# Optimization experiments

Measured on AMD Instinct MI355X. Metric: run time of the kernel, lower is better.

## Reference

```python
import jax, jax.numpy as jnp
import numpy as np

N = 50000      # nodes
E = 600000     # edges
D = 128        # inp_dim == emb_dim
R = 100        # num_rels
B = 4          # num_bases
L = 2          # num_layers
EPS = 1e-5


def setup_inputs() -> dict:
    key = jax.random.key(0)
    ks = jax.random.split(key, 4 + 6 * L)
    inp = {
        "feat": jax.random.normal(ks[0], (N, D), dtype=jnp.float32),
        "src": jax.random.randint(ks[1], (E,), 0, N),
        "dst": jax.random.randint(ks[2], (E,), 0, N),
        "etype": jax.random.randint(ks[3], (E,), 0, R),
    }
    for l in range(L):
        o = 4 + 6 * l
        s = 1.0 / np.sqrt(D)
        inp[f"V{l}"] = jax.random.normal(ks[o + 0], (B, D, D), dtype=jnp.float32) * s
        inp[f"comb{l}"] = jax.random.normal(ks[o + 1], (R, B), dtype=jnp.float32)
        inp[f"loop{l}"] = jax.random.normal(ks[o + 2], (D, D), dtype=jnp.float32) * s
        inp[f"bias{l}"] = jax.random.normal(ks[o + 3], (D,), dtype=jnp.float32) * 0.01
        inp[f"gamma{l}"] = jnp.ones((D,), dtype=jnp.float32)
        inp[f"beta{l}"] = jnp.zeros((D,), dtype=jnp.float32)
    return inp


def _rel_graph_conv(x, src, dst, etype, V, comb, W_loop, bias):
    # basis-decomposed relational conv: W_r = sum_b comb[r,b] * V[b]
    xb = jnp.einsum('nd,bdo->nbo', x, V)            # [N, B, D] project onto bases once
    msg = jnp.einsum('ebo,eb->eo', xb[src], comb[etype])  # [E, D] per-edge typed message
    agg = jax.ops.segment_sum(msg, dst, num_segments=N)   # scatter-add to destinations
    h = agg + x @ W_loop + bias                     # self-loop + bias (DGL defaults)
    return jax.nn.relu(h)


def _batch_norm(h, gamma, beta):
    mu = jnp.mean(h, axis=0)
    var = jnp.mean(jnp.square(h - mu), axis=0)      # biased var (training-mode BN)
    return gamma * (h - mu) * jax.lax.rsqrt(var + EPS) + beta


def reference(feat, src, dst, etype,
              V0, comb0, loop0, bias0, gamma0, beta0,
              V1, comb1, loop1, bias1, gamma1, beta1):
    h = feat
    h = _rel_graph_conv(h, src, dst, etype, V0, comb0, loop0, bias0)
    h = _batch_norm(h, gamma0, beta0)
    h = _rel_graph_conv(h, src, dst, etype, V1, comb1, loop1, bias1)
    h = _batch_norm(h, gamma1, beta1)
    return h  # JK='last'
```

## Files before the change

### kernel.cpp

```cpp
#include <hip/hip_runtime.h>
#include <hip/hip_bf16.h>

#define Nn 50000
#define Ee 600000
#define Dd 128
#define EPSc 1e-5f
#define GX 391

typedef unsigned int u32;
typedef unsigned short u16;
typedef short s16x8 __attribute__((ext_vector_type(8)));
typedef float f32x4 __attribute__((ext_vector_type(4)));

__device__ inline float bf2f(u32 lo16) { return __uint_as_float(lo16 << 16); }
__device__ inline u16 f2bf(float f) {
    u32 b = __float_as_uint(f);
    return (u16)((b + 0x7fffu + ((b >> 16) & 1u)) >> 16);
}
__device__ inline void gload16(const void* g, void* l) {
    __builtin_amdgcn_global_load_lds(
        (const __attribute__((address_space(1))) u32*)g,
        (__attribute__((address_space(3))) u32*)l, 16, 0, 0);
}

__global__ __launch_bounds__(256) void hist_k(const int* __restrict__ dst,
                                              int* __restrict__ cnt) {
    int e = blockIdx.x * 256 + threadIdx.x;
    if (e < Ee) atomicAdd(&cnt[dst[e]], 1);
}

__global__ __launch_bounds__(1024) void scan_k(const int* __restrict__ cnt,
                                               int* __restrict__ rowp) {
    __shared__ int wsum[16];
    __shared__ int carry_s;
    const int t = threadIdx.x, lane = t & 63, w = t >> 6;
    if (t == 0) { carry_s = 0; rowp[0] = 0; }
    __syncthreads();
    for (int base = 0; base < Nn; base += 1024) {
        int v = (base + t < Nn) ? cnt[base + t] : 0;
        int incl = v;
#pragma unroll
        for (int off = 1; off < 64; off <<= 1) {
            int u = __shfl_up(incl, off, 64);
            if (lane >= off) incl += u;
        }
        if (lane == 63) wsum[w] = incl;
        __syncthreads();
        if (t == 0) {
            int run = carry_s;
#pragma unroll
            for (int i = 0; i < 16; i++) { int s = wsum[i]; wsum[i] = run; run += s; }
            carry_s = run;
        }
        __syncthreads();
        if (base + t < Nn) rowp[base + t + 1] = wsum[w] + incl;
        __syncthreads();
    }
}

__global__ __launch_bounds__(256) void scatter_k(const int* __restrict__ src,
                                                 const int* __restrict__ dst,
                                                 const int* __restrict__ et,
                                                 int* __restrict__ cursor,
                                                 int2* __restrict__ se) {
    int e = blockIdx.x * 256 + threadIdx.x;
    if (e < Ee) {
        int pos = atomicAdd(&cursor[dst[e]], 1);
        se[pos] = make_int2(src[e], et[e]);
    }
}

__global__ __launch_bounds__(256) void conv_k(const float* __restrict__ in,
                                              u16* __restrict__ out) {
    const int total = Nn * 32;
    for (int i = blockIdx.x * 256 + threadIdx.x; i < total; i += gridDim.x * 256) {
        float4 v = ((const float4*)in)[i];
        ((ushort4*)out)[i] = make_ushort4(f2bf(v.x), f2bf(v.y), f2bf(v.z), f2bf(v.w));
    }
}

__global__ __launch_bounds__(256) void wprep_k(const float* __restrict__ V,
                                               const float* __restrict__ loop,
                                               u16* __restrict__ Wt) {
    int i = blockIdx.x * 256 + threadIdx.x;
    if (i >= 128 * 640) return;
    int c = i / 640, k = i - c * 640;
    float v = (k < 512) ? V[(size_t)k * 128 + c] : loop[(size_t)(k - 512) * 128 + c];
    Wt[i] = f2bf(v);
}

__global__ __launch_bounds__(256) void agg_k(const u16* __restrict__ x16,
                                             const int2* __restrict__ se,
                                             const int* __restrict__ rowp,
                                             const float* __restrict__ comb,
                                             u16* __restrict__ yb16) {
    const int node = blockIdx.x * 4 + (threadIdx.x >> 6);
    const int lane = threadIdx.x & 63;
    const int beg = rowp[node], end = rowp[node + 1];
    float a0x = 0.f, a0y = 0.f, a1x = 0.f, a1y = 0.f;
    float a2x = 0.f, a2y = 0.f, a3x = 0.f, a3y = 0.f;
    const int eL = end - 1;
    const int co = lane * 2;

    for (int e0 = beg; e0 < end; e0 += 4) {
        const int m = end - e0;
        const int2 rc0 = se[e0];
        const int2 rc1 = se[min(e0 + 1, eL)];
        const int2 rc2 = se[min(e0 + 2, eL)];
        const int2 rc3 = se[min(e0 + 3, eL)];
        u32 x0 = *(const u32*)&x16[(size_t)rc0.x * 128 + co];
        u32 x1 = *(const u32*)&x16[(size_t)rc1.x * 128 + co];
        u32 x2 = *(const u32*)&x16[(size_t)rc2.x * 128 + co];
        u32 x3 = *(const u32*)&x16[(size_t)rc3.x * 128 + co];
        if (m < 4) x3 = 0;
        if (m < 3) x2 = 0;
        if (m < 2) x1 = 0;
        const float4 c0 = ((const float4*)comb)[rc0.y];
        const float4 c1 = ((const float4*)comb)[rc1.y];
        const float4 c2 = ((const float4*)comb)[rc2.y];
        const float4 c3 = ((const float4*)comb)[rc3.y];
#define ACC1(c, xv)                                        \
        {                                                  \
            const float fx = bf2f((xv) & 0xffffu);         \
            const float fy = bf2f((xv) >> 16);             \
            a0x += c.x * fx; a0y += c.x * fy;              \
            a1x += c.y * fx; a1y += c.y * fy;              \
            a2x += c.z * fx; a2y += c.z * fy;              \
            a3x += c.w * fx; a3y += c.w * fy;              \
        }
        ACC1(c0, x0)
        ACC1(c1, x1)
        ACC1(c2, x2)
        ACC1(c3, x3)
#undef ACC1
    }
    u32* yp = (u32*)(yb16 + (size_t)node * 512);
    yp[lane]       = (u32)f2bf(a0x) | ((u32)f2bf(a0y) << 16);
    yp[64 + lane]  = (u32)f2bf(a1x) | ((u32)f2bf(a1y) << 16);
    yp[128 + lane] = (u32)f2bf(a2x) | ((u32)f2bf(a2y) << 16);
    yp[192 + lane] = (u32)f2bf(a3x) | ((u32)f2bf(a3y) << 16);
}

__global__ __launch_bounds__(256) void gemm_mfma_k(const u16* __restrict__ yb16,
                                                   const u16* __restrict__ x16,
                                                   const u16* __restrict__ Wt,
                                                   const float* __restrict__ bias,
                                                   float* __restrict__ OUT,
                                                   float* __restrict__ partials) {
    __shared__ __align__(16) char As[8192];
    __shared__ __align__(16) char Bs[8192];
    const int tid = threadIdx.x;
    const int lane = tid & 63, wid = tid >> 6;
    const int wr = wid >> 1, wc = wid & 1;
    const int bm = blockIdx.x * 128;

    f32x4 acc[4][4] = {};

    const int r0 = wid * 32;
    const int lrow = lane >> 2;
    const int sphys = lane & 3;
    const int rowL0 = r0 + lrow, rowL1 = r0 + 16 + lrow;
    const int slog0 = (sphys ^ ((rowL0 >> 1) & 3)) * 8;
    const int slog1 = (sphys ^ ((rowL1 >> 1) & 3)) * 8;
    int ga0 = bm + rowL0; if (ga0 >= Nn) ga0 = Nn - 1;
    int ga1 = bm + rowL1; if (ga1 >= Nn) ga1 = Nn - 1;

    for (int k0 = 0; k0 < 640; k0 += 32) {
        __syncthreads();
        const u16 *as0, *as1;
        if (k0 < 512) {
            as0 = yb16 + (size_t)ga0 * 512 + k0 + slog0;
            as1 = yb16 + (size_t)ga1 * 512 + k0 + slog1;
        } else {
            as0 = x16 + (size_t)ga0 * 128 + (k0 - 512) + slog0;
            as1 = x16 + (size_t)ga1 * 128 + (k0 - 512) + slog1;
        }
        gload16(as0, &As[r0 * 64]);
        gload16(as1, &As[(r0 + 16) * 64]);
        gload16(Wt + (size_t)rowL0 * 640 + k0 + slog0, &Bs[r0 * 64]);
        gload16(Wt + (size_t)rowL1 * 640 + k0 + slog1, &Bs[(r0 + 16) * 64]);
        __syncthreads();
        s16x8 a[4], b[4];
#pragma unroll
        for (int m = 0; m < 4; m++) {
            int row = wr * 64 + m * 16 + (lane & 15);
            a[m] = *(const s16x8*)&As[row * 64 + (((lane >> 4) ^ ((row >> 1) & 3)) << 4)];
            int col = wc * 64 + m * 16 + (lane & 15);
            b[m] = *(const s16x8*)&Bs[col * 64 + (((lane >> 4) ^ ((col >> 1) & 3)) << 4)];
        }
#pragma unroll
        for (int m = 0; m < 4; m++)
#pragma unroll
            for (int n = 0; n < 4; n++)
                acc[m][n] = __builtin_amdgcn_mfma_f32_16x16x32_bf16(a[m], b[n],
                                                                    acc[m][n], 0, 0, 0);
    }
    float bv[4], cs[4] = {}, cq[4] = {};
#pragma unroll
    for (int n = 0; n < 4; n++) bv[n] = bias[wc * 64 + n * 16 + (lane & 15)];
#pragma unroll
    for (int m = 0; m < 4; m++) {
        const int rb = bm + wr * 64 + m * 16 + ((lane >> 4) << 2);
#pragma unroll
        for (int e = 0; e < 4; e++) {
            const int r = rb + e;
            if (r < Nn) {
                float* op = OUT + (size_t)r * 128 + wc * 64 + (lane & 15);
#pragma unroll
                for (int n = 0; n < 4; n++) {
                    float v = fmaxf(acc[m][n][e] + bv[n], 0.f);
                    op[n * 16] = v;
                    cs[n] += v;
                    cq[n] += v * v;
                }
            }
        }
    }
#pragma unroll
    for (int n = 0; n < 4; n++) {
        cs[n] += __shfl_xor(cs[n], 16);
        cs[n] += __shfl_xor(cs[n], 32);
        cq[n] += __shfl_xor(cq[n], 16);
        cq[n] += __shfl_xor(cq[n], 32);
    }
    __syncthreads();
    float* red = (float*)As;
    if (wr == 1 && lane < 16) {
#pragma unroll
        for (int n = 0; n < 4; n++) {
            const int col = wc * 64 + n * 16 + lane;
            red[col] = cs[n];
            red[128 + col] = cq[n];
        }
    }
    __syncthreads();
    if (wr == 0 && lane < 16) {
        float* pp = partials + (size_t)blockIdx.x * 256;
#pragma unroll
        for (int n = 0; n < 4; n++) {
            const int col = wc * 64 + n * 16 + lane;
            pp[col] = cs[n] + red[col];
            pp[128 + col] = cq[n] + red[128 + col];
        }
    }
}

__global__ __launch_bounds__(256) void red_k(const float* __restrict__ partials,
                                             float* __restrict__ stats) {
    const int c = threadIdx.x;
    float s = 0.f;
    for (int b = blockIdx.x; b < GX; b += gridDim.x)
        s += partials[(size_t)b * 256 + c];
    unsafeAtomicAdd(&stats[c], s);
}

__global__ __launch_bounds__(256) void norm_k(const float* __restrict__ h,
                                              const float* __restrict__ stats,
                                              const float* __restrict__ gamma,
                                              const float* __restrict__ beta,
                                              float* __restrict__ out,
                                              u16* __restrict__ xb) {
    const float invN = 1.0f / (float)Nn;
    int total = Nn * 32;
    for (int i = blockIdx.x * blockDim.x + threadIdx.x; i < total;
         i += gridDim.x * blockDim.x) {
        int c = (i & 31) * 4;
        float4 v = ((const float4*)h)[i];
        float4 o;
        {
            float mu = stats[c + 0] * invN;
            float var = stats[Dd + c + 0] * invN - mu * mu;
            o.x = gamma[c + 0] * (v.x - mu) * rsqrtf(var + EPSc) + beta[c + 0];
        }
        {
            float mu = stats[c + 1] * invN;
            float var = stats[Dd + c + 1] * invN - mu * mu;
            o.y = gamma[c + 1] * (v.y - mu) * rsqrtf(var + EPSc) + beta[c + 1];
        }
        {
            float mu = stats[c + 2] * invN;
            float var = stats[Dd + c + 2] * invN - mu * mu;
            o.z = gamma[c + 2] * (v.z - mu) * rsqrtf(var + EPSc) + beta[c + 2];
        }
        {
            float mu = stats[c + 3] * invN;
            float var = stats[Dd + c + 3] * invN - mu * mu;
            o.w = gamma[c + 3] * (v.w - mu) * rsqrtf(var + EPSc) + beta[c + 3];
        }
        ((float4*)out)[i] = o;
        if (xb) ((ushort4*)xb)[i] = make_ushort4(f2bf(o.x), f2bf(o.y),
                                                 f2bf(o.z), f2bf(o.w));
    }
}

extern "C" void kernel_launch(void* const* d_in, const int* in_sizes, int n_in,
                              void* d_out, int out_size, void* d_ws, size_t ws_size,
                              hipStream_t stream) {
    const float* feat = (const float*)d_in[0];
    const int* src = (const int*)d_in[1];
    const int* dst = (const int*)d_in[2];
    const int* et = (const int*)d_in[3];
    float* out = (float*)d_out;

    char* p = (char*)d_ws;
    u16* yb16 = (u16*)p;     p += (size_t)Nn * 512 * 2;
    u16* x16 = (u16*)p;      p += (size_t)Nn * 128 * 2;
    u16* Wt = (u16*)p;       p += (size_t)128 * 640 * 2;
    int* rowp = (int*)p;     p += ((((size_t)(Nn + 1) * 4) + 15) & ~15ull);
    int2* se = (int2*)p;     p += (size_t)Ee * 8;
    float* partials = (float*)p;  p += (size_t)GX * 256 * 4;
    float* stats = (float*)p;
    int* cursor = (int*)yb16;

    hipMemsetAsync(cursor, 0, (size_t)Nn * 4, stream);
    hist_k<<<(Ee + 255) / 256, 256, 0, stream>>>(dst, cursor);
    scan_k<<<1, 1024, 0, stream>>>(cursor, rowp);
    hipMemcpyAsync(cursor, rowp, (size_t)Nn * 4, hipMemcpyDeviceToDevice, stream);
    scatter_k<<<(Ee + 255) / 256, 256, 0, stream>>>(src, dst, et, cursor, se);
    conv_k<<<1024, 256, 0, stream>>>(feat, x16);

    for (int l = 0; l < 2; l++) {
        const float* V = (const float*)d_in[4 + 6 * l + 0];
        const float* comb = (const float*)d_in[4 + 6 * l + 1];
        const float* loop = (const float*)d_in[4 + 6 * l + 2];
        const float* bias = (const float*)d_in[4 + 6 * l + 3];
        const float* gamma = (const float*)d_in[4 + 6 * l + 4];
        const float* beta = (const float*)d_in[4 + 6 * l + 5];

        wprep_k<<<(128 * 640 + 255) / 256, 256, 0, stream>>>(V, loop, Wt);
        agg_k<<<(Nn + 3) / 4, 256, 0, stream>>>(x16, se, rowp, comb, yb16);
        hipMemsetAsync(stats, 0, 2 * Dd * sizeof(float), stream);
        gemm_mfma_k<<<GX, 256, 0, stream>>>(yb16, x16, Wt, bias, out, partials);
        red_k<<<8, 256, 0, stream>>>(partials, stats);
        norm_k<<<2048, 256, 0, stream>>>(out, stats, gamma, beta, out,
                                         (l == 0) ? x16 : nullptr);
    }
}
```

Baseline: 317.4 us.

## Parallelize CSR prefix scan across blocks and unroll edge aggregation to eight

Replaces the single-block serial scan over 50000 node counts with a three-stage multi-block scan: per-block scans, a scan of the block sums, then an offset add. Separately, the aggregation loop gathers eight edges per iteration instead of four, and uses 32-bit index arithmetic, to put more independent loads in flight. This adds two extra kernel launches and raises register pressure in the aggregation kernel.

```diff
diff --git a/kernel.cpp b/kernel.cpp
--- a/kernel.cpp
+++ b/kernel.cpp
@@ -6,6 +6,7 @@
 #define Dd 128
 #define EPSc 1e-5f
 #define GX 391
+#define NB 196
 
 typedef unsigned int u32;
 typedef unsigned short u16;
@@ -29,33 +30,59 @@
     if (e < Ee) atomicAdd(&cnt[dst[e]], 1);
 }
 
-__global__ __launch_bounds__(1024) void scan_k(const int* __restrict__ cnt,
+__global__ __launch_bounds__(256) void scanA_k(const int* __restrict__ cnt,
+                                               int* __restrict__ rowp,
+                                               int* __restrict__ bsum) {
+    __shared__ int ws4[4];
+    const int tid = threadIdx.x, lane = tid & 63, w = tid >> 6;
+    const int i = blockIdx.x * 256 + tid;
+    int v = (i < Nn) ? cnt[i] : 0;
+    int incl = v;
+#pragma unroll
+    for (int off = 1; off < 64; off <<= 1) {
+        int u = __shfl_up(incl, off, 64);
+        if (lane >= off) incl += u;
+    }
+    if (lane == 63) ws4[w] = incl;
+    __syncthreads();
+    if (tid == 0) {
+        int run = 0;
+#pragma unroll
+        for (int j = 0; j < 4; j++) { int s = ws4[j]; ws4[j] = run; run += s; }
+    }
+    __syncthreads();
+    incl += ws4[w];
+    if (i < Nn) rowp[i + 1] = incl;
+    if (tid == 255) bsum[blockIdx.x] = incl;
+}
+
+__global__ __launch_bounds__(256) void scanB_k(const int* __restrict__ bsum,
+                                               int* __restrict__ boff) {
+    __shared__ int ws4[4];
+    const int tid = threadIdx.x, lane = tid & 63, w = tid >> 6;
+    int v = (tid < NB) ? bsum[tid] : 0;
+    int incl = v;
+#pragma unroll
+    for (int off = 1; off < 64; off <<= 1) {
+        int u = __shfl_up(incl, off, 64);
+        if (lane >= off) incl += u;
+    }
+    if (lane == 63) ws4[w] = incl;
+    __syncthreads();
+    if (tid == 0) {
+        int run = 0;
+#pragma unroll
+        for (int j = 0; j < 4; j++) { int s = ws4[j]; ws4[j] = run; run += s; }
+    }
+    __syncthreads();
+    if (tid < NB) boff[tid] = incl + ws4[w] - v;
+}
+
+__global__ __launch_bounds__(256) void scanC_k(const int* __restrict__ boff,
                                                int* __restrict__ rowp) {
-    __shared__ int wsum[16];
-    __shared__ int carry_s;
-    const int t = threadIdx.x, lane = t & 63, w = t >> 6;
-    if (t == 0) { carry_s = 0; rowp[0] = 0; }
-    __syncthreads();
-    for (int base = 0; base < Nn; base += 1024) {
-        int v = (base + t < Nn) ? cnt[base + t] : 0;
-        int incl = v;
-#pragma unroll
-        for (int off = 1; off < 64; off <<= 1) {
-            int u = __shfl_up(incl, off, 64);
-            if (lane >= off) incl += u;
-        }
-        if (lane == 63) wsum[w] = incl;
-        __syncthreads();
-        if (t == 0) {
-            int run = carry_s;
-#pragma unroll
-            for (int i = 0; i < 16; i++) { int s = wsum[i]; wsum[i] = run; run += s; }
-            carry_s = run;
-        }
-        __syncthreads();
-        if (base + t < Nn) rowp[base + t + 1] = wsum[w] + incl;
-        __syncthreads();
-    }
+    const int i = blockIdx.x * 256 + threadIdx.x;
+    if (i < Nn) rowp[i + 1] += boff[blockIdx.x];
+    if (i == 0) rowp[0] = 0;
 }
 
 __global__ __launch_bounds__(256) void scatter_k(const int* __restrict__ src,
@@ -100,39 +127,30 @@
     float a0x = 0.f, a0y = 0.f, a1x = 0.f, a1y = 0.f;
     float a2x = 0.f, a2y = 0.f, a3x = 0.f, a3y = 0.f;
     const int eL = end - 1;
-    const int co = lane * 2;
-
-    for (int e0 = beg; e0 < end; e0 += 4) {
+    const u32 co = (u32)lane * 2u;
+
+    for (int e0 = beg; e0 < end; e0 += 8) {
         const int m = end - e0;
-        const int2 rc0 = se[e0];
-        const int2 rc1 = se[min(e0 + 1, eL)];
-        const int2 rc2 = se[min(e0 + 2, eL)];
-        const int2 rc3 = se[min(e0 + 3, eL)];
-        u32 x0 = *(const u32*)&x16[(size_t)rc0.x * 128 + co];
-        u32 x1 = *(const u32*)&x16[(size_t)rc1.x * 128 + co];
-        u32 x2 = *(const u32*)&x16[(size_t)rc2.x * 128 + co];
-        u32 x3 = *(const u32*)&x16[(size_t)rc3.x * 128 + co];
-        if (m < 4) x3 = 0;
-        if (m < 3) x2 = 0;
-        if (m < 2) x1 = 0;
-        const float4 c0 = ((const float4*)comb)[rc0.y];
-        const float4 c1 = ((const float4*)comb)[rc1.y];
-        const float4 c2 = ((const float4*)comb)[rc2.y];
-        const float4 c3 = ((const float4*)comb)[rc3.y];
-#define ACC1(c, xv)                                        \
-        {                                                  \
-            const float fx = bf2f((xv) & 0xffffu);         \
-            const float fy = bf2f((xv) >> 16);             \
-            a0x += c.x * fx; a0y += c.x * fy;              \
-            a1x += c.y * fx; a1y += c.y * fy;              \
-            a2x += c.z * fx; a2y += c.z * fy;              \
-            a3x += c.w * fx; a3y += c.w * fy;              \
-        }
-        ACC1(c0, x0)
-        ACC1(c1, x1)
-        ACC1(c2, x2)
-        ACC1(c3, x3)
-#undef ACC1
+        int2 rc[8];
+        u32 xv[8];
+#pragma unroll
+        for (int j = 0; j < 8; j++) rc[j] = se[min(e0 + j, eL)];
+#pragma unroll
+        for (int j = 0; j < 8; j++)
+            xv[j] = *(const u32*)&x16[(u32)rc[j].x * 128u + co];
+#pragma unroll
+        for (int j = 1; j < 8; j++)
+            if (m <= j) xv[j] = 0;
+#pragma unroll
+        for (int j = 0; j < 8; j++) {
+            const float4 c = ((const float4*)comb)[rc[j].y];
+            const float fx = bf2f(xv[j] & 0xffffu);
+            const float fy = bf2f(xv[j] >> 16);
+            a0x += c.x * fx; a0y += c.x * fy;
+            a1x += c.y * fx; a1y += c.y * fy;
+            a2x += c.z * fx; a2y += c.z * fy;
+            a3x += c.w * fx; a3y += c.w * fy;
+        }
     }
     u32* yp = (u32*)(yb16 + (size_t)node * 512);
     yp[lane]       = (u32)f2bf(a0x) | ((u32)f2bf(a0y) << 16);
@@ -309,12 +327,16 @@
     int* rowp = (int*)p;     p += ((((size_t)(Nn + 1) * 4) + 15) & ~15ull);
     int2* se = (int2*)p;     p += (size_t)Ee * 8;
     float* partials = (float*)p;  p += (size_t)GX * 256 * 4;
-    float* stats = (float*)p;
+    float* stats = (float*)p;     p += 2 * Dd * 4;
+    int* bsum = (int*)p;          p += ((NB * 4 + 15) & ~15);
+    int* boff = (int*)p;          p += ((NB * 4 + 15) & ~15);
     int* cursor = (int*)yb16;
 
     hipMemsetAsync(cursor, 0, (size_t)Nn * 4, stream);
     hist_k<<<(Ee + 255) / 256, 256, 0, stream>>>(dst, cursor);
-    scan_k<<<1, 1024, 0, stream>>>(cursor, rowp);
+    scanA_k<<<NB, 256, 0, stream>>>(cursor, rowp, bsum);
+    scanB_k<<<1, 256, 0, stream>>>(bsum, boff);
+    scanC_k<<<NB, 256, 0, stream>>>(boff, rowp);
     hipMemcpyAsync(cursor, rowp, (size_t)Nn * 4, hipMemcpyDeviceToDevice, stream);
     scatter_k<<<(Ee + 255) / 256, 256, 0, stream>>>(src, dst, et, cursor, se);
     conv_k<<<1024, 256, 0, stream>>>(feat, x16);
```

Result: faster. 292.8 us (-7.7%).
